# Kernel tuning notes

Hardware: AMD Instinct MI355X
Metric: run time of the kernel (lower is better)

## Reference

```python
import jax, jax.numpy as jnp
import numpy as np

N_NODES = 32768
N_EDGES = 524288
EPS = 1e-5

def _layernorm(h):
    mu = jnp.mean(h, axis=-1, keepdims=True)
    var = jnp.var(h, axis=-1, keepdims=True)
    return (h - mu) / jnp.sqrt(var + EPS)

def _leaky_relu(h):
    return jnp.where(h >= 0, h, 0.01 * h)

def setup_inputs() -> dict:
    key = jax.random.key(0)
    ks = jax.random.split(key, 16)
    F, H, D = 256, 256, 1024
    x = jax.random.normal(ks[0], (N_NODES, F), dtype=jnp.float32)
    src = jax.random.randint(ks[1], (N_EDGES,), 0, N_NODES, dtype=jnp.int32)
    dst = jax.random.randint(ks[2], (N_EDGES,), 0, N_NODES, dtype=jnp.int32)
    dims = [F, H, H, H, D]
    params = {}
    for i in range(4):
        params[f"W{i+1}"] = jax.random.normal(ks[3 + i], (dims[i], dims[i + 1]), dtype=jnp.float32) * (1.0 / np.sqrt(dims[i]))
        params[f"b{i+1}"] = jnp.zeros((dims[i + 1],), dtype=jnp.float32)
    Wm = jax.random.normal(ks[8], (D, D), dtype=jnp.float32) * (1.0 / np.sqrt(D))
    bm = jnp.zeros((D,), dtype=jnp.float32)
    Ws = jax.random.normal(ks[9], (D, D), dtype=jnp.float32) * (1.0 / np.sqrt(D))
    bs = jnp.zeros((D,), dtype=jnp.float32)
    return dict(x=x, src=src, dst=dst, W1=params["W1"], b1=params["b1"], W2=params["W2"], b2=params["b2"], W3=params["W3"], b3=params["b3"], W4=params["W4"], b4=params["b4"], Wm=Wm, bm=bm, Ws=Ws, bs=bs, batch_b=128, nodes_per=256)

def reference(x, src, dst, W1, b1, W2, b2, W3, b3, W4, b4, Wm, bm, Ws, bs, batch_b, nodes_per):
    # DGL GraphConv norm='both': out = D_in^{-1/2} * A @ (D_out^{-1/2} * h) @ W + b
    ones = jnp.ones((src.shape[0],), dtype=x.dtype)
    out_deg = jax.ops.segment_sum(ones, src, num_segments=N_NODES)
    in_deg = jax.ops.segment_sum(ones, dst, num_segments=N_NODES)
    ns = jnp.where(out_deg > 0, jax.lax.rsqrt(out_deg), 1.0)[:, None]
    nd = jnp.where(in_deg > 0, jax.lax.rsqrt(in_deg), 1.0)[:, None]

    def gconv(h, W, b):
        if W.shape[0] <= W.shape[1]:  # aggregate first, then project (in <= out)
            m = (h * ns)[src]
            agg = jax.ops.segment_sum(m, dst, num_segments=N_NODES) * nd
            return agg @ W + b
        else:  # project first
            h = (h * ns) @ W
            agg = jax.ops.segment_sum(h[src], dst, num_segments=N_NODES) * nd
            return agg + b

    h = x
    for (W, b) in [(W1, b1), (W2, b2), (W3, b3), (W4, b4)]:
        h = _layernorm(_leaky_relu(gconv(h, W, b)))
    h = h.reshape(batch_b, nodes_per, -1)  # [B, N_per, D]
    h = jnp.mean(h, axis=1)                # AvePool over nodes
    h = _layernorm(h)
    mean = h @ Wm + bm
    log_std = h @ Ws + bs
    return (mean, log_std)
```

## Files before the change

### kernel.cpp

```cpp
#include <hip/hip_runtime.h>

#define N_NODES 32768
#define N_EDGES 524288

typedef __attribute__((ext_vector_type(8))) short short8;
typedef __attribute__((ext_vector_type(4))) float floatx4;

#define GLOBAL_AS __attribute__((address_space(1)))
#define LDS_AS __attribute__((address_space(3)))

__device__ __forceinline__ unsigned short f2bf(float x) {
    union { float f; unsigned u; } v; v.f = x;
    unsigned r = v.u + 0x7FFF + ((v.u >> 16) & 1);
    return (unsigned short)(r >> 16);
}
__device__ __forceinline__ float bf2f(unsigned short u) {
    union { unsigned u; float f; } v; v.u = ((unsigned)u) << 16;
    return v.f;
}


__global__ __launch_bounds__(256) void k_hist(const int* __restrict__ src,
                                              const int* __restrict__ dst,
                                              unsigned int* __restrict__ histOut32,
                                              unsigned int* __restrict__ histIn32) {
    __shared__ unsigned int hOut[8192];
    __shared__ unsigned int hIn[8192];
    int t = threadIdx.x, b = blockIdx.x;
    for (int i = t; i < 8192; i += 256) { hOut[i] = 0; hIn[i] = 0; }
    __syncthreads();
    int base = b * 4096;
    for (int i = t; i < 4096; i += 256) {
        int s = src[base + i], d = dst[base + i];
        atomicAdd(&hOut[s >> 2], 1u << ((s & 3) * 8));
        atomicAdd(&hIn[d >> 2], 1u << ((d & 3) * 8));
    }
    __syncthreads();
    for (int i = t; i < 8192; i += 256) {
        histOut32[b * 8192 + i] = hOut[i];
        histIn32[b * 8192 + i] = hIn[i];
    }
}

__global__ __launch_bounds__(256) void k_merge_p1(const unsigned int* __restrict__ histIn32,
                                                  const unsigned int* __restrict__ histOut32,
                                                  unsigned int* __restrict__ partIn,
                                                  unsigned int* __restrict__ partOut) {
    int g = blockIdx.x * 256 + threadIdx.x;
    int bg = blockIdx.y;
    unsigned int si = 0, so = 0;
#pragma unroll
    for (int j = 0; j < 16; j++) {
        si += histIn32[(bg * 16 + j) * 8192 + g];
        so += histOut32[(bg * 16 + j) * 8192 + g];
    }
    partIn[bg * 8192 + g] = si;
    partOut[bg * 8192 + g] = so;
}

__global__ __launch_bounds__(256) void k_merge_p2(const unsigned int* __restrict__ histIn32,
                                                  const unsigned int* __restrict__ partIn,
                                                  const unsigned int* __restrict__ partOut,
                                                  unsigned int* __restrict__ pre32,
                                                  int* __restrict__ in_deg,
                                                  float* __restrict__ ns,
                                                  float* __restrict__ nd) {
    int g = blockIdx.x * 256 + threadIdx.x;
    int bg = blockIdx.y;
    unsigned int run = 0;
    for (int b2 = 0; b2 < bg; b2++) run += partIn[b2 * 8192 + g];
    for (int j = 0; j < 16; j++) {
        int b = bg * 16 + j;
        pre32[b * 8192 + g] = run;
        run += histIn32[b * 8192 + g];
    }
    if (bg == 7) {
        int r0 = run & 255, r1 = (run >> 8) & 255, r2 = (run >> 16) & 255, r3 = (run >> 24) & 255;
        in_deg[g * 4 + 0] = r0; in_deg[g * 4 + 1] = r1;
        in_deg[g * 4 + 2] = r2; in_deg[g * 4 + 3] = r3;
        nd[g * 4 + 0] = r0 > 0 ? rsqrtf((float)r0) : 1.0f;
        nd[g * 4 + 1] = r1 > 0 ? rsqrtf((float)r1) : 1.0f;
        nd[g * 4 + 2] = r2 > 0 ? rsqrtf((float)r2) : 1.0f;
        nd[g * 4 + 3] = r3 > 0 ? rsqrtf((float)r3) : 1.0f;
    }
    if (bg == 0) {
        unsigned int to = 0;
#pragma unroll
        for (int b2 = 0; b2 < 8; b2++) to += partOut[b2 * 8192 + g];
        int r0 = to & 255, r1 = (to >> 8) & 255, r2 = (to >> 16) & 255, r3 = (to >> 24) & 255;
        ns[g * 4 + 0] = r0 > 0 ? rsqrtf((float)r0) : 1.0f;
        ns[g * 4 + 1] = r1 > 0 ? rsqrtf((float)r1) : 1.0f;
        ns[g * 4 + 2] = r2 > 0 ? rsqrtf((float)r2) : 1.0f;
        ns[g * 4 + 3] = r3 > 0 ? rsqrtf((float)r3) : 1.0f;
    }
}

__global__ __launch_bounds__(256) void k_scanA(const int* __restrict__ in_deg,
                                               int* __restrict__ row_ptr,
                                               int* __restrict__ blkSum) {
    __shared__ int part[256];
    int t = threadIdx.x, b = blockIdx.x;
    int base = (b * 256 + t) * 4;
    int l0 = in_deg[base], l1 = in_deg[base + 1], l2 = in_deg[base + 2], l3 = in_deg[base + 3];
    part[t] = l0 + l1 + l2 + l3;
    __syncthreads();
    for (int off = 1; off < 256; off <<= 1) {
        int v = (t >= off) ? part[t - off] : 0;
        __syncthreads();
        part[t] += v;
        __syncthreads();
    }
    int excl = (t == 0) ? 0 : part[t - 1];
    row_ptr[base] = excl;
    row_ptr[base + 1] = excl + l0;
    row_ptr[base + 2] = excl + l0 + l1;
    row_ptr[base + 3] = excl + l0 + l1 + l2;
    if (t == 255) blkSum[b] = part[255];
}

__global__ __launch_bounds__(256) void k_scanC(const int* __restrict__ blkSum,
                                               int* __restrict__ row_ptr) {
    __shared__ int soff;
    int t = threadIdx.x, b = blockIdx.x;
    if (t == 0) {
        int s = 0;
        for (int i = 0; i < b; i++) s += blkSum[i];
        soff = s;
    }
    __syncthreads();
    int base = (b * 256 + t) * 4;
    row_ptr[base] += soff; row_ptr[base + 1] += soff;
    row_ptr[base + 2] += soff; row_ptr[base + 3] += soff;
    if (b == 31 && t == 255) row_ptr[N_NODES] = soff + blkSum[31];
}

__global__ __launch_bounds__(256) void k_place(const int* __restrict__ src,
                                               const int* __restrict__ dst,
                                               const unsigned int* __restrict__ pre32,
                                               const int* __restrict__ row_ptr,
                                               int* __restrict__ csr_src) {
    __shared__ unsigned int cur[8192];
    int t = threadIdx.x, b = blockIdx.x;
    for (int i = t; i < 8192; i += 256) cur[i] = 0;
    __syncthreads();
    int base = b * 4096;
    const unsigned int* preb = pre32 + b * 8192;
    for (int i = t; i < 4096; i += 256) {
        int s = src[base + i], d = dst[base + i];
        int sh = (d & 3) * 8;
        unsigned int old = atomicAdd(&cur[d >> 2], 1u << sh);
        int rank = (old >> sh) & 255;
        int pb = (preb[d >> 2] >> sh) & 255;
        csr_src[row_ptr[d] + pb + rank] = s;
    }
}

struct TransDescs {
    const float* W[6];
    unsigned short* Wt[6];
    int K[6], N[6];
    int end[6];
};

__global__ __launch_bounds__(256) void k_transpose_all(TransDescs d) {
    int id = blockIdx.x, s = 0;
#pragma unroll
    for (int i = 0; i < 6; i++) if (id >= d.end[i]) s = i + 1;
    int base = (s == 0) ? 0 : d.end[s - 1];
    int t = id - base;
    int K = d.K[s], N = d.N[s];
    int ncols = N >> 5;
    int n0 = (t % ncols) * 32, k0 = (t / ncols) * 32;
    const float* W = d.W[s];
    unsigned short* Wt = d.Wt[s];
    __shared__ float tile[32][33];
    int tx = threadIdx.x & 31, ty = threadIdx.x >> 5;
    for (int r = 0; r < 32; r += 8)
        tile[ty + r][tx] = W[(size_t)(k0 + ty + r) * N + n0 + tx];
    __syncthreads();
    for (int r = 0; r < 32; r += 8)
        Wt[(size_t)(n0 + ty + r) * K + k0 + tx] = f2bf(tile[tx][ty + r]);
}

__global__ __launch_bounds__(256) void k_scale_x(const float* __restrict__ x,
                                                 const float* __restrict__ ns,
                                                 unsigned short* __restrict__ xsb) {
    int i = blockIdx.x * 256 + threadIdx.x;
    float4 v = ((const float4*)x)[i];
    int n = i >> 6;
    int f = (i & 63) * 4;
    float sc = ns[n];
    ushort4 o;
    o.x = f2bf(v.x * sc); o.y = f2bf(v.y * sc);
    o.z = f2bf(v.z * sc); o.w = f2bf(v.w * sc);
    size_t off = (size_t)(f >> 6) * (N_NODES * 64) + (size_t)n * 64 + (f & 63);
    *(ushort4*)(xsb + off) = o;
}

__global__ __launch_bounds__(512, 4) void fused_layer(
        const unsigned short* __restrict__ hs,
        const int* __restrict__ row_ptr,
        const int* __restrict__ csr_src,
        const float* __restrict__ nd,
        const unsigned short* __restrict__ Bt,
        const float* __restrict__ bias,
        const float* __restrict__ ns,
        unsigned short* __restrict__ ho) {
    __shared__ __align__(16) unsigned short At[8 * 2048];
    __shared__ __align__(16) unsigned short Bs[2][256 * 32];
    __shared__ int eIdx[2048];
    __shared__ int rp[65];
    __shared__ float sSum[4][64], sSum2[4][64], sMa[64], sMb[64];
    const int tid = threadIdx.x;
    const int lane = tid & 63;
    const int w = tid >> 6;
    const int n0 = blockIdx.x * 64;
    const int K = 256;

    const int pr = lane >> 3;
    const int uu = (lane & 7) ^ pr;
    const int rowInGrp = pr * 2 + (uu >> 2);
    const int kc = (uu & 3) * 8;
    const unsigned short* gB = Bt + (size_t)(w * 32 + rowInGrp) * K + kc;
    const int bBase = (w * 32) * 32;
#define STAGEB(buf_, koff_)                                                              \
    {                                                                                    \
        unsigned short* lB = Bs[buf_] + bBase;                                           \
        __builtin_amdgcn_global_load_lds((const GLOBAL_AS short*)(gB + (koff_)),         \
                                         (LDS_AS short*)lB, 16, 0, 0);                   \
        __builtin_amdgcn_global_load_lds((const GLOBAL_AS short*)(gB + (koff_) + (size_t)16 * K), \
                                         (LDS_AS short*)(lB + 16 * 32), 16, 0, 0);       \
    }
    STAGEB(0, 0)

    if (tid <= 64) rp[tid] = row_ptr[n0 + tid];
    __syncthreads();
    const int ebeg = rp[0];
    const int ecount = rp[64] - ebeg;
    const int ecached = ecount < 2048 ? ecount : 2048;
    for (int i = tid; i < ecached; i += 512) eIdx[i] = csr_src[ebeg + i];
    __syncthreads();

    const int r = tid >> 3;
    const int fs = tid & 7;
    const int beg = rp[r] - ebeg, end = rp[r + 1] - ebeg;
    const float sc = nd[n0 + r];
    const int rowpair = r >> 1;
    unsigned short* atp = At + rowpair * 64 +
                          (((((r & 1) << 2) | (fs & 3)) ^ (rowpair & 7)) << 3);

    auto sweep = [&](auto fetch) {
        for (int c = 0; c < 4; c++) {
            const unsigned short* hp = hs + (size_t)c * (N_NODES * 64) + fs * 8;
            float acc[8];
#pragma unroll
            for (int k = 0; k < 8; k++) acc[k] = 0.f;
            int e = beg;
            for (; e + 8 <= end; e += 8) {
                int s0 = fetch(e),     s1 = fetch(e + 1), s2 = fetch(e + 2), s3 = fetch(e + 3);
                int s4 = fetch(e + 4), s5 = fetch(e + 5), s6 = fetch(e + 6), s7 = fetch(e + 7);
                short8 v0 = *(const short8*)(hp + (size_t)s0 * 64);
                short8 v1 = *(const short8*)(hp + (size_t)s1 * 64);
                short8 v2 = *(const short8*)(hp + (size_t)s2 * 64);
                short8 v3 = *(const short8*)(hp + (size_t)s3 * 64);
                short8 v4 = *(const short8*)(hp + (size_t)s4 * 64);
                short8 v5 = *(const short8*)(hp + (size_t)s5 * 64);
                short8 v6 = *(const short8*)(hp + (size_t)s6 * 64);
                short8 v7 = *(const short8*)(hp + (size_t)s7 * 64);
#pragma unroll
                for (int k = 0; k < 8; k++)
                    acc[k] += ((bf2f((unsigned short)v0[k]) + bf2f((unsigned short)v1[k])) +
                               (bf2f((unsigned short)v2[k]) + bf2f((unsigned short)v3[k]))) +
                              ((bf2f((unsigned short)v4[k]) + bf2f((unsigned short)v5[k])) +
                               (bf2f((unsigned short)v6[k]) + bf2f((unsigned short)v7[k])));
            }
            for (; e + 2 <= end; e += 2) {
                int s0 = fetch(e), s1 = fetch(e + 1);
                short8 v0 = *(const short8*)(hp + (size_t)s0 * 64);
                short8 v1 = *(const short8*)(hp + (size_t)s1 * 64);
#pragma unroll
                for (int k = 0; k < 8; k++)
                    acc[k] += bf2f((unsigned short)v0[k]) + bf2f((unsigned short)v1[k]);
            }
            if (e < end) {
                int s = fetch(e);
                short8 v = *(const short8*)(hp + (size_t)s * 64);
#pragma unroll
                for (int k = 0; k < 8; k++) acc[k] += bf2f((unsigned short)v[k]);
            }
            short8 o;
#pragma unroll
            for (int k = 0; k < 8; k++) o[k] = (short)f2bf(acc[k] * sc);
            *(short8*)(atp + (c * 2 + (fs >> 2)) * 2048) = o;
        }
    };
    if (ecount <= 2048)
        sweep([&](int e) { return eIdx[e]; });
    else
        sweep([&](int e) { return csr_src[ebeg + e]; });

    const int wr = (w >> 2) * 32;
    const int wc = (w & 3) * 64;
    floatx4 acc2[2][4];
#pragma unroll
    for (int i = 0; i < 2; i++)
#pragma unroll
        for (int j = 0; j < 4; j++) acc2[i][j] = (floatx4){0.f, 0.f, 0.f, 0.f};
    const int q = lane >> 4;
    const int ln = lane & 15;
    const int uf = (((ln & 1) << 2) | q) ^ ((ln >> 1) & 7);

    int buf = 0;
    for (int k0 = 0; k0 < K; k0 += 32) {
        __syncthreads();
        if (k0 + 32 < K) STAGEB(buf ^ 1, k0 + 32)
        const unsigned short* rA = At + (k0 >> 5) * 2048;
        const unsigned short* rB = Bs[buf];
        short8 af[2], bfr[4];
#pragma unroll
        for (int i = 0; i < 2; i++)
            af[i] = *(const short8*)(rA + (((wr + i * 16 + ln) >> 1) << 6) + uf * 8);
#pragma unroll
        for (int j = 0; j < 4; j++)
            bfr[j] = *(const short8*)(rB + (((wc + j * 16 + ln) >> 1) << 6) + uf * 8);
#pragma unroll
        for (int i = 0; i < 2; i++)
#pragma unroll
            for (int j = 0; j < 4; j++)
                acc2[i][j] = __builtin_amdgcn_mfma_f32_16x16x32_bf16(af[i], bfr[j], acc2[i][j], 0, 0, 0);
        buf ^= 1;
    }
#undef STAGEB

    float bcol[4];
#pragma unroll
    for (int j = 0; j < 4; j++) bcol[j] = bias[wc + j * 16 + ln];
    const int wcIdx = w & 3;
#pragma unroll
    for (int i = 0; i < 2; i++) {
#pragma unroll
        for (int rr = 0; rr < 4; rr++) {
            float s = 0.f, s2 = 0.f;
#pragma unroll
            for (int j = 0; j < 4; j++) {
                float v = acc2[i][j][rr] + bcol[j];
                v = v >= 0.f ? v : 0.01f * v;
                s += v; s2 += v * v;
            }
#pragma unroll
            for (int off = 8; off > 0; off >>= 1) {
                s += __shfl_down(s, off, 16);
                s2 += __shfl_down(s2, off, 16);
            }
            if (ln == 0) {
                int row = wr + i * 16 + q * 4 + rr;
                sSum[wcIdx][row] = s;
                sSum2[wcIdx][row] = s2;
            }
        }
    }
    __syncthreads();
    if (tid < 64) {
        float su = sSum[0][tid] + sSum[1][tid] + sSum[2][tid] + sSum[3][tid];
        float su2 = sSum2[0][tid] + sSum2[1][tid] + sSum2[2][tid] + sSum2[3][tid];
        float mu = su * (1.0f / 256.0f);
        float var = su2 * (1.0f / 256.0f) - mu * mu;
        float rs = rsqrtf(var + 1e-5f);
        float nsv = ns[n0 + tid];
        sMa[tid] = rs * nsv;
        sMb[tid] = -mu * rs * nsv;
    }
    __syncthreads();
#pragma unroll
    for (int i = 0; i < 2; i++) {
#pragma unroll
        for (int rr = 0; rr < 4; rr++) {
            int row = wr + i * 16 + q * 4 + rr;
            float a = sMa[row], bb = sMb[row];
#pragma unroll
            for (int j = 0; j < 4; j++) {
                float v = acc2[i][j][rr] + bcol[j];
                v = v >= 0.f ? v : 0.01f * v;
                int col = wc + j * 16 + ln;
                size_t off = (size_t)(col >> 6) * (N_NODES * 64) +
                             (size_t)(n0 + row) * 64 + (col & 63);
                ho[off] = f2bf(v * a + bb);
            }
        }
    }
}

__global__ __launch_bounds__(512, 4) void fused_layer4(
        const unsigned short* __restrict__ hs,
        const int* __restrict__ row_ptr,
        const int* __restrict__ csr_src,
        const float* __restrict__ nd,
        const unsigned short* __restrict__ Bt,
        const float* __restrict__ bias,
        unsigned short* __restrict__ h4) {
    __shared__ __align__(16) unsigned short At[8 * 2048];
    __shared__ __align__(16) unsigned short Bs[2][256 * 32];
    __shared__ int eIdx[2048];
    __shared__ int rp[65];
    const int tid = threadIdx.x;
    const int lane = tid & 63;
    const int w = tid >> 6;
    const int n0 = blockIdx.x * 64;
    const int K = 256;

    const int pr = lane >> 3;
    const int uu = (lane & 7) ^ pr;
    const int rowInGrp = pr * 2 + (uu >> 2);
    const int kc = (uu & 3) * 8;
    const int bBase = (w * 32) * 32;
#define STAGEB4(buf_, ct_, koff_)                                                        \
    {                                                                                    \
        const unsigned short* gB = Bt + (size_t)((ct_) * 256 + w * 32 + rowInGrp) * K + kc; \
        unsigned short* lB = Bs[buf_] + bBase;                                           \
        __builtin_amdgcn_global_load_lds((const GLOBAL_AS short*)(gB + (koff_)),         \
                                         (LDS_AS short*)lB, 16, 0, 0);                   \
        __builtin_amdgcn_global_load_lds((const GLOBAL_AS short*)(gB + (koff_) + (size_t)16 * K), \
                                         (LDS_AS short*)(lB + 16 * 32), 16, 0, 0);       \
    }
    STAGEB4(0, 0, 0)

    if (tid <= 64) rp[tid] = row_ptr[n0 + tid];
    __syncthreads();
    const int ebeg = rp[0];
    const int ecount = rp[64] - ebeg;
    const int ecached = ecount < 2048 ? ecount : 2048;
    for (int i = tid; i < ecached; i += 512) eIdx[i] = csr_src[ebeg + i];
    __syncthreads();

    const int r = tid >> 3;
    const int fs = tid & 7;
    const int beg = rp[r] - ebeg, end = rp[r + 1] - ebeg;
    const float sc = nd[n0 + r];
    const int rowpair = r >> 1;
    unsigned short* atp = At + rowpair * 64 +
                          (((((r & 1) << 2) | (fs & 3)) ^ (rowpair & 7)) << 3);

    auto sweep = [&](auto fetch) {
#pragma unroll
        for (int cp = 0; cp < 2; cp++) {
            const unsigned short* hpA = hs + (size_t)(cp * 2) * (N_NODES * 64) + fs * 8;
            const unsigned short* hpB = hpA + (size_t)N_NODES * 64;
            float accA[8], accB[8];
#pragma unroll
            for (int k = 0; k < 8; k++) { accA[k] = 0.f; accB[k] = 0.f; }
            int e = beg;
            for (; e + 8 <= end; e += 8) {
                int s0 = fetch(e),     s1 = fetch(e + 1), s2 = fetch(e + 2), s3 = fetch(e + 3);
                int s4 = fetch(e + 4), s5 = fetch(e + 5), s6 = fetch(e + 6), s7 = fetch(e + 7);
                short8 a0 = *(const short8*)(hpA + (size_t)s0 * 64);
                short8 a1 = *(const short8*)(hpA + (size_t)s1 * 64);
                short8 a2 = *(const short8*)(hpA + (size_t)s2 * 64);
                short8 a3 = *(const short8*)(hpA + (size_t)s3 * 64);
                short8 a4 = *(const short8*)(hpA + (size_t)s4 * 64);
                short8 a5 = *(const short8*)(hpA + (size_t)s5 * 64);
                short8 a6 = *(const short8*)(hpA + (size_t)s6 * 64);
                short8 a7 = *(const short8*)(hpA + (size_t)s7 * 64);
                short8 b0 = *(const short8*)(hpB + (size_t)s0 * 64);
                short8 b1 = *(const short8*)(hpB + (size_t)s1 * 64);
                short8 b2 = *(const short8*)(hpB + (size_t)s2 * 64);
                short8 b3 = *(const short8*)(hpB + (size_t)s3 * 64);
                short8 b4 = *(const short8*)(hpB + (size_t)s4 * 64);
                short8 b5 = *(const short8*)(hpB + (size_t)s5 * 64);
                short8 b6 = *(const short8*)(hpB + (size_t)s6 * 64);
                short8 b7 = *(const short8*)(hpB + (size_t)s7 * 64);
#pragma unroll
                for (int k = 0; k < 8; k++) {
                    accA[k] += ((bf2f((unsigned short)a0[k]) + bf2f((unsigned short)a1[k])) +
                                (bf2f((unsigned short)a2[k]) + bf2f((unsigned short)a3[k]))) +
                               ((bf2f((unsigned short)a4[k]) + bf2f((unsigned short)a5[k])) +
                                (bf2f((unsigned short)a6[k]) + bf2f((unsigned short)a7[k])));
                    accB[k] += ((bf2f((unsigned short)b0[k]) + bf2f((unsigned short)b1[k])) +
                                (bf2f((unsigned short)b2[k]) + bf2f((unsigned short)b3[k]))) +
                               ((bf2f((unsigned short)b4[k]) + bf2f((unsigned short)b5[k])) +
                                (bf2f((unsigned short)b6[k]) + bf2f((unsigned short)b7[k])));
                }
            }
            for (; e + 2 <= end; e += 2) {
                int s0 = fetch(e), s1 = fetch(e + 1);
                short8 a0 = *(const short8*)(hpA + (size_t)s0 * 64);
                short8 a1 = *(const short8*)(hpA + (size_t)s1 * 64);
                short8 b0 = *(const short8*)(hpB + (size_t)s0 * 64);
                short8 b1 = *(const short8*)(hpB + (size_t)s1 * 64);
#pragma unroll
                for (int k = 0; k < 8; k++) {
                    accA[k] += bf2f((unsigned short)a0[k]) + bf2f((unsigned short)a1[k]);
                    accB[k] += bf2f((unsigned short)b0[k]) + bf2f((unsigned short)b1[k]);
                }
            }
            if (e < end) {
                int s = fetch(e);
                short8 a0 = *(const short8*)(hpA + (size_t)s * 64);
                short8 b0 = *(const short8*)(hpB + (size_t)s * 64);
#pragma unroll
                for (int k = 0; k < 8; k++) {
                    accA[k] += bf2f((unsigned short)a0[k]);
                    accB[k] += bf2f((unsigned short)b0[k]);
                }
            }
            short8 oA, oB;
#pragma unroll
            for (int k = 0; k < 8; k++) {
                oA[k] = (short)f2bf(accA[k] * sc);
                oB[k] = (short)f2bf(accB[k] * sc);
            }
            *(short8*)(atp + ((cp * 2) * 2 + (fs >> 2)) * 2048) = oA;
            *(short8*)(atp + ((cp * 2 + 1) * 2 + (fs >> 2)) * 2048) = oB;
        }
    };
    if (ecount <= 2048)
        sweep([&](int e) { return eIdx[e]; });
    else
        sweep([&](int e) { return csr_src[ebeg + e]; });

    const int wr = (w >> 2) * 32;
    const int wc = (w & 3) * 64;
    const int q = lane >> 4;
    const int ln = lane & 15;
    const int uf = (((ln & 1) << 2) | q) ^ ((ln >> 1) & 7);

    int buf = 0;
    for (int ct = 0; ct < 4; ct++) {
        floatx4 acc2[2][4];
#pragma unroll
        for (int i = 0; i < 2; i++)
#pragma unroll
            for (int j = 0; j < 4; j++) acc2[i][j] = (floatx4){0.f, 0.f, 0.f, 0.f};
        for (int k0 = 0; k0 < K; k0 += 32) {
            __syncthreads();
            if (k0 + 32 < K) {
                STAGEB4(buf ^ 1, ct, k0 + 32)
            } else if (ct < 3) {
                STAGEB4(buf ^ 1, ct + 1, 0)
            }
            const unsigned short* rA = At + (k0 >> 5) * 2048;
            const unsigned short* rB = Bs[buf];
            short8 af[2], bfr[4];
#pragma unroll
            for (int i = 0; i < 2; i++)
                af[i] = *(const short8*)(rA + (((wr + i * 16 + ln) >> 1) << 6) + uf * 8);
#pragma unroll
            for (int j = 0; j < 4; j++)
                bfr[j] = *(const short8*)(rB + (((wc + j * 16 + ln) >> 1) << 6) + uf * 8);
#pragma unroll
            for (int i = 0; i < 2; i++)
#pragma unroll
                for (int j = 0; j < 4; j++)
                    acc2[i][j] = __builtin_amdgcn_mfma_f32_16x16x32_bf16(af[i], bfr[j], acc2[i][j], 0, 0, 0);
            buf ^= 1;
        }
#pragma unroll
        for (int i = 0; i < 2; i++) {
#pragma unroll
            for (int rr = 0; rr < 4; rr++) {
                int row = wr + i * 16 + q * 4 + rr;
#pragma unroll
                for (int j = 0; j < 4; j++) {
                    int col = ct * 256 + wc + j * 16 + ln;
                    float v = acc2[i][j][rr] + bias[col];
                    v = v >= 0.f ? v : 0.01f * v;
                    h4[(size_t)(n0 + row) * 1024 + col] = f2bf(v);
                }
            }
        }
    }
#undef STAGEB4
}

__global__ __launch_bounds__(256) void gemm_heads(
        const unsigned short* __restrict__ A,
        const unsigned short* __restrict__ Bt,
        float* __restrict__ P) {
    __shared__ __align__(16) unsigned short As[2][128 * 32];
    __shared__ __align__(16) unsigned short Bs[2][128 * 32];
    const int tid = threadIdx.x;
    const int lane = tid & 63;
    const int w = tid >> 6;
    const int wr = (w >> 1) * 64;
    const int wc = (w & 1) * 64;
    const int colBase = blockIdx.x * 128;
    const int ks = blockIdx.y;
    const int K = 1024;

    floatx4 acc[4][4];
#pragma unroll
    for (int i = 0; i < 4; i++)
#pragma unroll
        for (int j = 0; j < 4; j++) acc[i][j] = (floatx4){0.f, 0.f, 0.f, 0.f};

    const int pr = lane >> 3;
    const int uu = (lane & 7) ^ pr;
    const int srow = w * 32 + pr * 2 + (uu >> 2);
    const int kc = (uu & 3) * 8;
    const unsigned short* gA = A + (size_t)srow * K + ks * 128 + kc;
    const unsigned short* gB = Bt + (size_t)(colBase + srow) * K + ks * 128 + kc;
    const int wbase = (w * 32) * 32;

    const int q = lane >> 4;
    const int ln = lane & 15;
    const int uf = (((ln & 1) << 2) | q) ^ ((ln >> 1) & 7);

    {
        unsigned short* lA = As[0] + wbase;
        unsigned short* lB = Bs[0] + wbase;
        __builtin_amdgcn_global_load_lds((const GLOBAL_AS short*)(gA),
                                         (LDS_AS short*)lA, 16, 0, 0);
        __builtin_amdgcn_global_load_lds((const GLOBAL_AS short*)(gA + (size_t)16 * K),
                                         (LDS_AS short*)(lA + 16 * 32), 16, 0, 0);
        __builtin_amdgcn_global_load_lds((const GLOBAL_AS short*)(gB),
                                         (LDS_AS short*)lB, 16, 0, 0);
        __builtin_amdgcn_global_load_lds((const GLOBAL_AS short*)(gB + (size_t)16 * K),
                                         (LDS_AS short*)(lB + 16 * 32), 16, 0, 0);
    }

    int buf = 0;
    for (int k0 = 0; k0 < 128; k0 += 32) {
        __syncthreads();
        if (k0 + 32 < 128) {
            unsigned short* lA = As[buf ^ 1] + wbase;
            unsigned short* lB = Bs[buf ^ 1] + wbase;
            __builtin_amdgcn_global_load_lds((const GLOBAL_AS short*)(gA + k0 + 32),
                                             (LDS_AS short*)lA, 16, 0, 0);
            __builtin_amdgcn_global_load_lds((const GLOBAL_AS short*)(gA + k0 + 32 + (size_t)16 * K),
                                             (LDS_AS short*)(lA + 16 * 32), 16, 0, 0);
            __builtin_amdgcn_global_load_lds((const GLOBAL_AS short*)(gB + k0 + 32),
                                             (LDS_AS short*)lB, 16, 0, 0);
            __builtin_amdgcn_global_load_lds((const GLOBAL_AS short*)(gB + k0 + 32 + (size_t)16 * K),
                                             (LDS_AS short*)(lB + 16 * 32), 16, 0, 0);
        }
        const unsigned short* rA = As[buf];
        const unsigned short* rB = Bs[buf];
        short8 af[4], bfr[4];
#pragma unroll
        for (int i = 0; i < 4; i++)
            af[i] = *(const short8*)(rA + (((wr + i * 16 + ln) >> 1) << 6) + uf * 8);
#pragma unroll
        for (int j = 0; j < 4; j++)
            bfr[j] = *(const short8*)(rB + (((wc + j * 16 + ln) >> 1) << 6) + uf * 8);
#pragma unroll
        for (int i = 0; i < 4; i++)
#pragma unroll
            for (int j = 0; j < 4; j++)
                acc[i][j] = __builtin_amdgcn_mfma_f32_16x16x32_bf16(af[i], bfr[j], acc[i][j], 0, 0, 0);
        buf ^= 1;
    }
    float* Pk = P + (size_t)ks * 128 * 2048;
#pragma unroll
    for (int i = 0; i < 4; i++) {
#pragma unroll
        for (int j = 0; j < 4; j++) {
#pragma unroll
            for (int r = 0; r < 4; r++) {
                int row = wr + i * 16 + q * 4 + r;
                int col = colBase + wc + j * 16 + ln;
                Pk[(size_t)row * 2048 + col] = acc[i][j][r];
            }
        }
    }
}

__global__ __launch_bounds__(256) void k_heads_reduce(
        const float* __restrict__ P, const float* __restrict__ bm,
        const float* __restrict__ bsd, float* __restrict__ out) {
    int idx = blockIdx.x * 256 + threadIdx.x;
    int row = idx >> 9;
    int col = (idx & 511) * 4;
    floatx4 s = (floatx4){0.f, 0.f, 0.f, 0.f};
#pragma unroll
    for (int p = 0; p < 8; p++)
        s += *(const floatx4*)(P + (size_t)p * 128 * 2048 + (size_t)row * 2048 + col);
    bool hi = col >= 1024;
    const float* bias = hi ? bsd : bm;
    int bc = hi ? col - 1024 : col;
    s += *(const floatx4*)(bias + bc);
    float* o = hi ? (out + (size_t)128 * 1024 + (size_t)row * 1024 + bc)
                  : (out + (size_t)row * 1024 + col);
    *(floatx4*)o = s;
}

__global__ __launch_bounds__(256) void k_lnpool(const unsigned short* __restrict__ h4,
                                                float* __restrict__ partial) {
    const int g = blockIdx.y, p = blockIdx.x;
    const int w = threadIdx.x >> 6, lane = threadIdx.x & 63;
    float acc[16];
#pragma unroll
    for (int k = 0; k < 16; k++) acc[k] = 0.f;
    for (int i = 0; i < 8; i++) {
        int node = (g * 8 + p) * 32 + w * 8 + i;
        const unsigned short* row = h4 + (size_t)node * 1024 + lane * 16;
        short8 a = *(const short8*)row;
        short8 b = *(const short8*)(row + 8);
        float v[16];
#pragma unroll
        for (int k = 0; k < 8; k++) v[k] = bf2f((unsigned short)a[k]);
#pragma unroll
        for (int k = 0; k < 8; k++) v[8 + k] = bf2f((unsigned short)b[k]);
        float s = 0.f, s2 = 0.f;
#pragma unroll
        for (int k = 0; k < 16; k++) { s += v[k]; s2 += v[k] * v[k]; }
#pragma unroll
        for (int off = 32; off > 0; off >>= 1) {
            s += __shfl_down(s, off);
            s2 += __shfl_down(s2, off);
        }
        s = __shfl(s, 0);
        s2 = __shfl(s2, 0);
        float mu = s * (1.0f / 1024.0f);
        float var = s2 * (1.0f / 1024.0f) - mu * mu;
        float rs = rsqrtf(var + 1e-5f);
#pragma unroll
        for (int k = 0; k < 16; k++) acc[k] += (v[k] - mu) * rs;
    }
    __shared__ float red[4][1024];
    float* my = red[w] + lane * 16;
#pragma unroll
    for (int k = 0; k < 16; k++) my[k] = acc[k];
    __syncthreads();
    int t = threadIdx.x;
    floatx4 o = (floatx4){0.f, 0.f, 0.f, 0.f};
#pragma unroll
    for (int w2 = 0; w2 < 4; w2++) {
        const floatx4 v = *(const floatx4*)(red[w2] + t * 4);
        o += v;
    }
    __builtin_nontemporal_store(o, (floatx4*)(partial + (size_t)(g * 8 + p) * 1024 + t * 4));
}

__global__ __launch_bounds__(256) void k_pool_final(const float* __restrict__ partial,
                                                    unsigned short* __restrict__ pooledb) {
    int g = blockIdx.x, t = threadIdx.x;
    int wave = t >> 6;
    float4 a = make_float4(0.f, 0.f, 0.f, 0.f);
    for (int p = 0; p < 8; p++) {
        float4 v = *(const float4*)(partial + (size_t)(g * 8 + p) * 1024 + t * 4);
        a.x += v.x; a.y += v.y; a.z += v.z; a.w += v.w;
    }
    const float invn = 1.0f / 256.0f;
    a.x *= invn; a.y *= invn; a.z *= invn; a.w *= invn;
    float s = a.x + a.y + a.z + a.w;
    float s2 = a.x * a.x + a.y * a.y + a.z * a.z + a.w * a.w;
#pragma unroll
    for (int off = 32; off > 0; off >>= 1) {
        s += __shfl_down(s, off);
        s2 += __shfl_down(s2, off);
    }
    __shared__ float ss[4], ss2[4];
    if ((t & 63) == 0) { ss[wave] = s; ss2[wave] = s2; }
    __syncthreads();
    if (t == 0) {
        float tt = 0.f, tt2 = 0.f;
        for (int w = 0; w < 4; w++) { tt += ss[w]; tt2 += ss2[w]; }
        float mu = tt / 1024.f;
        float var = tt2 / 1024.f - mu * mu;
        ss[0] = mu;
        ss2[0] = rsqrtf(var + 1e-5f);
    }
    __syncthreads();
    float mu = ss[0], inv = ss2[0];
    ushort4 o;
    o.x = f2bf((a.x - mu) * inv); o.y = f2bf((a.y - mu) * inv);
    o.z = f2bf((a.z - mu) * inv); o.w = f2bf((a.w - mu) * inv);
    *(ushort4*)(pooledb + (size_t)g * 1024 + t * 4) = o;
}

extern "C" void kernel_launch(void* const* d_in, const int* in_sizes, int n_in,
                              void* d_out, int out_size, void* d_ws, size_t ws_size,
                              hipStream_t stream) {
    const float* x  = (const float*)d_in[0];
    const int*   src = (const int*)d_in[1];
    const int*   dst = (const int*)d_in[2];
    const float* W1 = (const float*)d_in[3];  const float* b1 = (const float*)d_in[4];
    const float* W2 = (const float*)d_in[5];  const float* b2 = (const float*)d_in[6];
    const float* W3 = (const float*)d_in[7];  const float* b3 = (const float*)d_in[8];
    const float* W4 = (const float*)d_in[9];  const float* b4 = (const float*)d_in[10];
    const float* Wm = (const float*)d_in[11]; const float* bm = (const float*)d_in[12];
    const float* Wsd = (const float*)d_in[13]; const float* bsd = (const float*)d_in[14];
    float* out = (float*)d_out;

    char* w = (char*)d_ws;
    unsigned short* hsbA = (unsigned short*)w; w += (size_t)N_NODES * 256 * 2;
    unsigned short* hsbB = (unsigned short*)w; w += (size_t)N_NODES * 256 * 2;
    unsigned short* h4b  = (unsigned short*)w; w += (size_t)N_NODES * 1024 * 2;
    float* partial = (float*)w; w += (size_t)128 * 8 * 1024 * 4;
    unsigned short* pooledb = (unsigned short*)w; w += (size_t)128 * 1024 * 2;
    unsigned short* W1t = (unsigned short*)w; w += (size_t)256 * 256 * 2;
    unsigned short* W2t = (unsigned short*)w; w += (size_t)256 * 256 * 2;
    unsigned short* W3t = (unsigned short*)w; w += (size_t)256 * 256 * 2;
    unsigned short* W4t = (unsigned short*)w; w += (size_t)256 * 1024 * 2;
    unsigned short* Wmt = (unsigned short*)w; w += (size_t)1024 * 1024 * 2;
    unsigned short* Wst = (unsigned short*)w; w += (size_t)1024 * 1024 * 2;
    float* ns     = (float*)w; w += (size_t)N_NODES * 4;
    float* nd     = (float*)w; w += (size_t)N_NODES * 4;
    unsigned int* histOut32 = (unsigned int*)w; w += (size_t)128 * 8192 * 4;
    unsigned int* histIn32  = (unsigned int*)w; w += (size_t)128 * 8192 * 4;
    unsigned int* pre32     = (unsigned int*)w; w += (size_t)128 * 8192 * 4;
    unsigned int* partIn    = (unsigned int*)w; w += (size_t)8 * 8192 * 4;
    unsigned int* partOut   = (unsigned int*)w; w += (size_t)8 * 8192 * 4;
    int* blkSum   = (int*)w;   w += (size_t)64 * 4;
    int* in_deg   = (int*)w;   w += (size_t)N_NODES * 4;
    int* row_ptr  = (int*)w;   w += (size_t)(N_NODES + 1) * 4;
    int* csr_src  = (int*)w;   w += (size_t)N_EDGES * 4;
    float* headp = (float*)histOut32;

    TransDescs td;
    td.W[0] = W1; td.W[1] = W2; td.W[2] = W3; td.W[3] = W4; td.W[4] = Wm; td.W[5] = Wsd;
    td.Wt[0] = W1t; td.Wt[1] = W2t; td.Wt[2] = W3t; td.Wt[3] = W4t; td.Wt[4] = Wmt; td.Wt[5] = Wst;
    td.K[0] = 256; td.K[1] = 256; td.K[2] = 256; td.K[3] = 256; td.K[4] = 1024; td.K[5] = 1024;
    td.N[0] = 256; td.N[1] = 256; td.N[2] = 256; td.N[3] = 1024; td.N[4] = 1024; td.N[5] = 1024;
    td.end[0] = 64; td.end[1] = 128; td.end[2] = 192; td.end[3] = 448; td.end[4] = 1472; td.end[5] = 2496;
    k_transpose_all<<<2496, 256, 0, stream>>>(td);

    k_hist<<<128, 256, 0, stream>>>(src, dst, histOut32, histIn32);
    k_merge_p1<<<dim3(32, 8), 256, 0, stream>>>(histIn32, histOut32, partIn, partOut);
    k_merge_p2<<<dim3(32, 8), 256, 0, stream>>>(histIn32, partIn, partOut, pre32, in_deg, ns, nd);
    k_scanA<<<32, 256, 0, stream>>>(in_deg, row_ptr, blkSum);
    k_scanC<<<32, 256, 0, stream>>>(blkSum, row_ptr);
    k_place<<<128, 256, 0, stream>>>(src, dst, pre32, row_ptr, csr_src);

    k_scale_x<<<N_NODES * 256 / 1024, 256, 0, stream>>>(x, ns, hsbA);

    const unsigned short* Wts[3] = {W1t, W2t, W3t};
    const float* bs3[3] = {b1, b2, b3};
    unsigned short* tin = hsbA;
    unsigned short* tout = hsbB;
    for (int l = 0; l < 3; l++) {
        fused_layer<<<N_NODES / 64, 512, 0, stream>>>(tin, row_ptr, csr_src, nd,
                                                      Wts[l], bs3[l], ns, tout);
        unsigned short* tmp = tin; tin = tout; tout = tmp;
    }

    fused_layer4<<<N_NODES / 64, 512, 0, stream>>>(tin, row_ptr, csr_src, nd,
                                                   W4t, b4, h4b);

    k_lnpool<<<dim3(8, 128), 256, 0, stream>>>(h4b, partial);
    k_pool_final<<<128, 256, 0, stream>>>(partial, pooledb);

    gemm_heads<<<dim3(16, 8), 256, 0, stream>>>(pooledb, Wmt, headp);
    k_heads_reduce<<<256, 256, 0, stream>>>(headp, bm, bsd, out);
}
```

Before: 339.3 us.

## Fuse final layernorm and mean-pool partial sums into layer-4 kernel epilogue

The separate k_lnpool kernel is removed. fused_layer4 now gathers per-row sum and sum-of-squares statistics of its bf16 outputs through shuffles and LDS. It then re-reads its own 64 rows of h4, applies the layernorm and writes a per-block pooled partial, so k_pool_final sums 4 partials per graph instead of 8. This saves a kernel launch and the standalone full pass that recomputed row statistics, at the cost of extra LDS atomics-free accumulation, syncs and a re-read of h4 (likely cache-resident) inside an already heavy kernel.

```diff
diff --git a/kernel.cpp b/kernel.cpp
--- a/kernel.cpp
+++ b/kernel.cpp
@@ -5,6 +5,7 @@
 
 typedef __attribute__((ext_vector_type(8))) short short8;
 typedef __attribute__((ext_vector_type(4))) float floatx4;
+typedef __attribute__((ext_vector_type(2))) float floatx2;
 
 #define GLOBAL_AS __attribute__((address_space(1)))
 #define LDS_AS __attribute__((address_space(3)))
@@ -397,11 +398,13 @@
         const float* __restrict__ nd,
         const unsigned short* __restrict__ Bt,
         const float* __restrict__ bias,
-        unsigned short* __restrict__ h4) {
+        unsigned short* __restrict__ h4,
+        float* __restrict__ partial) {
     __shared__ __align__(16) unsigned short At[8 * 2048];
     __shared__ __align__(16) unsigned short Bs[2][256 * 32];
     __shared__ int eIdx[2048];
     __shared__ int rp[65];
+    __shared__ float sS[4][64], sS2[4][64];
     const int tid = threadIdx.x;
     const int lane = tid & 63;
     const int w = tid >> 6;
@@ -425,6 +428,10 @@
     STAGEB4(0, 0, 0)
 
     if (tid <= 64) rp[tid] = row_ptr[n0 + tid];
+    if (tid < 64) {
+#pragma unroll
+        for (int w2 = 0; w2 < 4; w2++) { sS[w2][tid] = 0.f; sS2[w2][tid] = 0.f; }
+    }
     __syncthreads();
     const int ebeg = rp[0];
     const int ecount = rp[64] - ebeg;
@@ -522,6 +529,7 @@
     const int q = lane >> 4;
     const int ln = lane & 15;
     const int uf = (((ln & 1) << 2) | q) ^ ((ln >> 1) & 7);
+    const int wcIdx = w & 3;
 
     int buf = 0;
     for (int ct = 0; ct < 4; ct++) {
@@ -558,17 +566,71 @@
 #pragma unroll
             for (int rr = 0; rr < 4; rr++) {
                 int row = wr + i * 16 + q * 4 + rr;
+                float s = 0.f, s2 = 0.f;
 #pragma unroll
                 for (int j = 0; j < 4; j++) {
                     int col = ct * 256 + wc + j * 16 + ln;
                     float v = acc2[i][j][rr] + bias[col];
                     v = v >= 0.f ? v : 0.01f * v;
-                    h4[(size_t)(n0 + row) * 1024 + col] = f2bf(v);
+                    unsigned short u = f2bf(v);
+                    h4[(size_t)(n0 + row) * 1024 + col] = u;
+                    float vr = bf2f(u);
+                    s += vr; s2 += vr * vr;
                 }
+#pragma unroll
+                for (int off = 8; off > 0; off >>= 1) {
+                    s += __shfl_down(s, off, 16);
+                    s2 += __shfl_down(s2, off, 16);
+                }
+                if (ln == 0) {
+                    sS[wcIdx][row] += s;
+                    sS2[wcIdx][row] += s2;
+                }
             }
         }
     }
 #undef STAGEB4
+
+    __syncthreads();
+    if (tid < 64) {
+        float tot = sS[0][tid] + sS[1][tid] + sS[2][tid] + sS[3][tid];
+        float tot2 = sS2[0][tid] + sS2[1][tid] + sS2[2][tid] + sS2[3][tid];
+        float mu = tot * (1.0f / 1024.0f);
+        float var = tot2 * (1.0f / 1024.0f) - mu * mu;
+        sS[0][tid] = mu;
+        sS2[0][tid] = rsqrtf(var + 1e-5f);
+    }
+    __syncthreads();
+
+    float accp[16];
+#pragma unroll
+    for (int k = 0; k < 16; k++) accp[k] = 0.f;
+    for (int i = 0; i < 8; i++) {
+        int nl = w * 8 + i;
+        const unsigned short* rowp = h4 + (size_t)(n0 + nl) * 1024 + lane * 16;
+        short8 a = *(const short8*)rowp;
+        short8 b = *(const short8*)(rowp + 8);
+        float mu = sS[0][nl], rs = sS2[0][nl];
+#pragma unroll
+        for (int k = 0; k < 8; k++) accp[k] += (bf2f((unsigned short)a[k]) - mu) * rs;
+#pragma unroll
+        for (int k = 0; k < 8; k++) accp[8 + k] += (bf2f((unsigned short)b[k]) - mu) * rs;
+    }
+    float* red = (float*)At;
+    float* my = red + w * 1024 + lane * 16;
+#pragma unroll
+    for (int k = 0; k < 16; k++) my[k] = accp[k];
+    __syncthreads();
+    {
+        int c = tid * 2;
+        floatx2 o = (floatx2){0.f, 0.f};
+#pragma unroll
+        for (int w2 = 0; w2 < 8; w2++) {
+            o[0] += red[w2 * 1024 + c];
+            o[1] += red[w2 * 1024 + c + 1];
+        }
+        __builtin_nontemporal_store(o, (floatx2*)(partial + (size_t)blockIdx.x * 1024 + c));
+    }
 }
 
 __global__ __launch_bounds__(256) void gemm_heads(
@@ -682,61 +744,13 @@
     *(floatx4*)o = s;
 }
 
-__global__ __launch_bounds__(256) void k_lnpool(const unsigned short* __restrict__ h4,
-                                                float* __restrict__ partial) {
-    const int g = blockIdx.y, p = blockIdx.x;
-    const int w = threadIdx.x >> 6, lane = threadIdx.x & 63;
-    float acc[16];
-#pragma unroll
-    for (int k = 0; k < 16; k++) acc[k] = 0.f;
-    for (int i = 0; i < 8; i++) {
-        int node = (g * 8 + p) * 32 + w * 8 + i;
-        const unsigned short* row = h4 + (size_t)node * 1024 + lane * 16;
-        short8 a = *(const short8*)row;
-        short8 b = *(const short8*)(row + 8);
-        float v[16];
-#pragma unroll
-        for (int k = 0; k < 8; k++) v[k] = bf2f((unsigned short)a[k]);
-#pragma unroll
-        for (int k = 0; k < 8; k++) v[8 + k] = bf2f((unsigned short)b[k]);
-        float s = 0.f, s2 = 0.f;
-#pragma unroll
-        for (int k = 0; k < 16; k++) { s += v[k]; s2 += v[k] * v[k]; }
-#pragma unroll
-        for (int off = 32; off > 0; off >>= 1) {
-            s += __shfl_down(s, off);
-            s2 += __shfl_down(s2, off);
-        }
-        s = __shfl(s, 0);
-        s2 = __shfl(s2, 0);
-        float mu = s * (1.0f / 1024.0f);
-        float var = s2 * (1.0f / 1024.0f) - mu * mu;
-        float rs = rsqrtf(var + 1e-5f);
-#pragma unroll
-        for (int k = 0; k < 16; k++) acc[k] += (v[k] - mu) * rs;
-    }
-    __shared__ float red[4][1024];
-    float* my = red[w] + lane * 16;
-#pragma unroll
-    for (int k = 0; k < 16; k++) my[k] = acc[k];
-    __syncthreads();
-    int t = threadIdx.x;
-    floatx4 o = (floatx4){0.f, 0.f, 0.f, 0.f};
-#pragma unroll
-    for (int w2 = 0; w2 < 4; w2++) {
-        const floatx4 v = *(const floatx4*)(red[w2] + t * 4);
-        o += v;
-    }
-    __builtin_nontemporal_store(o, (floatx4*)(partial + (size_t)(g * 8 + p) * 1024 + t * 4));
-}
-
 __global__ __launch_bounds__(256) void k_pool_final(const float* __restrict__ partial,
                                                     unsigned short* __restrict__ pooledb) {
     int g = blockIdx.x, t = threadIdx.x;
     int wave = t >> 6;
     float4 a = make_float4(0.f, 0.f, 0.f, 0.f);
-    for (int p = 0; p < 8; p++) {
-        float4 v = *(const float4*)(partial + (size_t)(g * 8 + p) * 1024 + t * 4);
+    for (int p = 0; p < 4; p++) {
+        float4 v = *(const float4*)(partial + (size_t)(g * 4 + p) * 1024 + t * 4);
         a.x += v.x; a.y += v.y; a.z += v.z; a.w += v.w;
     }
     const float invn = 1.0f / 256.0f;
@@ -785,7 +799,7 @@
     unsigned short* hsbA = (unsigned short*)w; w += (size_t)N_NODES * 256 * 2;
     unsigned short* hsbB = (unsigned short*)w; w += (size_t)N_NODES * 256 * 2;
     unsigned short* h4b  = (unsigned short*)w; w += (size_t)N_NODES * 1024 * 2;
-    float* partial = (float*)w; w += (size_t)128 * 8 * 1024 * 4;
+    float* partial = (float*)w; w += (size_t)512 * 1024 * 4;
     unsigned short* pooledb = (unsigned short*)w; w += (size_t)128 * 1024 * 2;
     unsigned short* W1t = (unsigned short*)w; w += (size_t)256 * 256 * 2;
     unsigned short* W2t = (unsigned short*)w; w += (size_t)256 * 256 * 2;
@@ -834,9 +848,8 @@
     }
 
     fused_layer4<<<N_NODES / 64, 512, 0, stream>>>(tin, row_ptr, csr_src, nd,
-                                                   W4t, b4, h4b);
-
-    k_lnpool<<<dim3(8, 128), 256, 0, stream>>>(h4b, partial);
+                                                   W4t, b4, h4b, partial);
+
     k_pool_final<<<128, 256, 0, stream>>>(partial, pooledb);
 
     gemm_heads<<<dim3(16, 8), 256, 0, stream>>>(pooledb, Wmt, headp);
```

After: 342.0 us. Within noise of the previous version (+0.8%).
